# Kernel tuning notes

Hardware: AMD Instinct MI355X
Metric: run time of the kernel (lower is better)

The kernel has to match this reference:

```python
import jax, jax.numpy as jnp
import numpy as np
import math

HEADS = 16
HIDDEN = 2048
D_K = HIDDEN // HEADS
BATCH = 2
SEQ = 2048
ROPE_THETA = 10000.0


def make_freqs_cis(seq_len, d_k, theta=ROPE_THETA):
    # Llama rotary frequencies; returned as (seq, d_k//2, 2) = (cos, sin)
    inv_freq = 1.0 / (theta ** (np.arange(0, d_k, 2, dtype=np.float32) / d_k))
    t = np.arange(seq_len, dtype=np.float32)
    ang = np.outer(t, inv_freq)  # (seq, d_k//2)
    return jnp.asarray(np.stack([np.cos(ang), np.sin(ang)], axis=-1))


def setup_inputs() -> dict:
    key = jax.random.key(0)
    ks = jax.random.split(key, 5)
    scale = 1.0 / math.sqrt(HIDDEN)
    return {
        "x": jax.random.normal(ks[0], (BATCH, SEQ, HIDDEN), dtype=jnp.float32),
        "freqs_cis": make_freqs_cis(SEQ, D_K),
        "wq": jax.random.normal(ks[1], (HIDDEN, HIDDEN), dtype=jnp.float32) * scale,
        "wk": jax.random.normal(ks[2], (HIDDEN, HIDDEN), dtype=jnp.float32) * scale,
        "wv": jax.random.normal(ks[3], (HIDDEN, HIDDEN), dtype=jnp.float32) * scale,
        "wo": jax.random.normal(ks[4], (HIDDEN, HIDDEN), dtype=jnp.float32) * scale,
    }


def _apply_rope(t, cos, sin):
    # t: (B, S, h, d_k); cos/sin: (1, S, 1, d_k//2)
    B, S, h, dk = t.shape
    tp = t.reshape(B, S, h, dk // 2, 2)
    t0, t1 = tp[..., 0], tp[..., 1]
    r0 = t0 * cos - t1 * sin
    r1 = t0 * sin + t1 * cos
    return jnp.stack([r0, r1], axis=-1).reshape(B, S, h, dk)


def reference(x, freqs_cis, wq, wk, wv, wo):
    B, S, H = x.shape
    h, dk = HEADS, H // HEADS
    # nn.Linear(bias=False): y = x @ W.T
    q = (x @ wq.T).reshape(B, S, h, dk)
    k = (x @ wk.T).reshape(B, S, h, dk)
    v = (x @ wv.T).reshape(B, S, h, dk)
    cos = freqs_cis[None, :, None, :, 0]
    sin = freqs_cis[None, :, None, :, 1]
    q = _apply_rope(q, cos, sin)
    k = _apply_rope(k, cos, sin)
    # (B, h, S, dk)
    q = q.transpose(0, 2, 1, 3)
    k = k.transpose(0, 2, 1, 3)
    v = v.transpose(0, 2, 1, 3)
    scores = jnp.einsum("bhqd,bhkd->bhqk", q, k) / math.sqrt(dk)
    causal = jnp.tril(jnp.ones((S, S), dtype=bool))
    scores = jnp.where(causal[None, None], scores, -jnp.inf)
    attn = jax.nn.softmax(scores, axis=-1)
    out = jnp.einsum("bhqk,bhkd->bhqd", attn, v)
    out = out.transpose(0, 2, 1, 3).reshape(B, S, H)
    return out @ wo.T
```

## Files before the change

### kernel.cpp

```cpp
#include <hip/hip_runtime.h>

#define SEQ 2048
#define HID 2048
#define NH 16
#define DK 128
#define NTOK 4096

typedef __bf16 bf16x8 __attribute__((ext_vector_type(8)));
typedef float f32x4 __attribute__((ext_vector_type(4)));
typedef float f32x16 __attribute__((ext_vector_type(16)));
typedef unsigned int u32x4 __attribute__((ext_vector_type(4)));

__device__ __forceinline__ unsigned short f2bf(float f) {
  unsigned int u = __builtin_bit_cast(unsigned int, f);
  u += 0x7fffu + ((u >> 16) & 1u);
  return (unsigned short)(u >> 16);
}
__device__ __forceinline__ float bf2f(unsigned int lo16) {
  return __builtin_bit_cast(float, lo16 << 16);
}

__device__ __forceinline__ void async_cp16(const void* g, void* l) {
  __builtin_amdgcn_global_load_lds(
      (__attribute__((address_space(1))) void*)const_cast<void*>(g),
      (__attribute__((address_space(3))) void*)l, 16, 0, 0);
}

__global__ void convert_all_kernel(const float* __restrict__ x,
                                   const float* __restrict__ wq,
                                   const float* __restrict__ wk,
                                   const float* __restrict__ wv,
                                   const float* __restrict__ wo,
                                   const float* __restrict__ fc,
                                   unsigned short* __restrict__ xb,
                                   unsigned short* __restrict__ wqb,
                                   unsigned short* __restrict__ wkb,
                                   unsigned short* __restrict__ wvb,
                                   unsigned short* __restrict__ wob,
                                   unsigned int* __restrict__ fcb) {
  const int bid = blockIdx.x;
  if (bid >= 24576) {
    const int idx = (bid - 24576) * 256 + threadIdx.x;
    const int s = idx >> 6, d = idx & 63;
    const float2 cs = *(const float2*)(fc + s * 128 + 2 * d);
    fcb[idx] = (unsigned int)f2bf(cs.x) | ((unsigned int)f2bf(cs.y) << 16);
    return;
  }
  const float* src;
  unsigned short* dst;
  int base;
  if (bid < 8192) {
    src = x; dst = xb; base = bid;
  } else {
    const int t = (bid - 8192) >> 12;
    base = (bid - 8192) & 4095;
    src = (t == 0) ? wq : (t == 1) ? wk : (t == 2) ? wv : wo;
    dst = (t == 0) ? wqb : (t == 1) ? wkb : (t == 2) ? wvb : wob;
  }
  const int i = base * 256 + threadIdx.x;
  float4 v = ((const float4*)src)[i];
  ushort4 o;
  o.x = f2bf(v.x); o.y = f2bf(v.y); o.z = f2bf(v.z); o.w = f2bf(v.w);
  ((ushort4*)dst)[i] = o;
}

template<bool F32OUT>
__global__ __launch_bounds__(256, 2)
void gemm_bt_kernel(const unsigned short* __restrict__ A,
                    const unsigned short* __restrict__ B,
                    unsigned short* __restrict__ Ob,
                    float* __restrict__ Of,
                    const unsigned int* __restrict__ fcb,
                    const int mode) {
  __shared__ alignas(16) unsigned short As[128 * 64];
  __shared__ alignas(16) unsigned short Bs[128 * 64];

  const int bx = blockIdx.x, by = blockIdx.y;
  const int col0 = bx * 128;
  const int row0 = by * 128;

  const int tid = threadIdx.x;
  const int wave = tid >> 6, lane = tid & 63;
  const int quad = lane >> 4, r = lane & 15;
  const int wm = wave >> 1, wn = wave & 1;
  const int jbase = wave * 256 + lane;

  f32x4 acc[4][4] = {};

  for (int k0 = 0; k0 < HID; k0 += 64) {
    for (int t = 0; t < 4; ++t) {
      const int j = jbase + t * 64;
      const int m = j >> 3;
      const int gc = (j & 7) ^ (m & 7);
      async_cp16(A + (size_t)(row0 + m) * HID + k0 + gc * 8, As + j * 8);
      async_cp16(B + (size_t)(col0 + m) * HID + k0 + gc * 8, Bs + j * 8);
    }
    __syncthreads();
    for (int kk = 0; kk < 2; ++kk) {
      bf16x8 af[4], bfr[4];
      for (int mt = 0; mt < 4; ++mt) {
        const int m = wm * 64 + mt * 16 + r;
        const int slot = (kk * 4 + quad) ^ (m & 7);
        af[mt] = __builtin_bit_cast(bf16x8, *(const u32x4*)(As + m * 64 + slot * 8));
      }
      for (int nt = 0; nt < 4; ++nt) {
        const int n = wn * 64 + nt * 16 + r;
        const int slot = (kk * 4 + quad) ^ (n & 7);
        bfr[nt] = __builtin_bit_cast(bf16x8, *(const u32x4*)(Bs + n * 64 + slot * 8));
      }
      for (int mt = 0; mt < 4; ++mt)
        for (int nt = 0; nt < 4; ++nt)
          acc[mt][nt] = __builtin_amdgcn_mfma_f32_16x16x32_bf16(
              af[mt], bfr[nt], acc[mt][nt], 0, 0, 0);
    }
    __syncthreads();
  }

  if (!F32OUT && mode == 2) {
    for (int mt = 0; mt < 4; ++mt) {
      const int row = row0 + wm * 64 + mt * 16 + quad * 4;
      const int b = row >> 11, s = row & (SEQ - 1);
      for (int nt = 0; nt < 4; ++nt) {
        const int col = col0 + wn * 64 + nt * 16 + r;
        ushort4 pk;
        pk.x = f2bf(acc[mt][nt][0]);
        pk.y = f2bf(acc[mt][nt][1]);
        pk.z = f2bf(acc[mt][nt][2]);
        pk.w = f2bf(acc[mt][nt][3]);
        *(ushort4*)(Ob + ((size_t)(b * HID + col)) * SEQ + s) = pk;
      }
    }
    return;
  }

  if (!F32OUT) {
    const float qs = (mode == 0) ? 0.12751743f : 1.0f;
    for (int mt = 0; mt < 4; ++mt) {
      const int row = row0 + wm * 64 + mt * 16 + quad * 4;
      for (int nt = 0; nt < 4; ++nt) {
        const int col = col0 + wn * 64 + nt * 16 + r;
        const int d = (wn * 64 + nt * 16 + r) >> 1;
        for (int v = 0; v < 4; ++v) {
          const int s = (row + v) & (SEQ - 1);
          const unsigned int u = fcb[s * 64 + d];
          const float c = bf2f(u & 0xffffu), sn = bf2f(u >> 16);
          const float val = acc[mt][nt][v];
          const float par = __shfl_xor(val, 1, 64);
          const float res = (r & 1) ? (par * sn + val * c)
                                    : (val * c - par * sn);
          Ob[(size_t)(row + v) * HID + col] = f2bf(res * qs);
        }
      }
    }
    return;
  }

  for (int mt = 0; mt < 4; ++mt) {
    const int row = row0 + wm * 64 + mt * 16 + quad * 4;
    for (int nt = 0; nt < 4; ++nt) {
      const int col = col0 + wn * 64 + nt * 16 + r;
      for (int v = 0; v < 4; ++v)
        Of[(size_t)(row + v) * HID + col] = acc[mt][nt][v];
    }
  }
}

__global__ __launch_bounds__(256, 2)
void flash_attn_kernel(const unsigned short* __restrict__ Qb,
                       const unsigned short* __restrict__ Kb,
                       const unsigned short* __restrict__ VtG,
                       unsigned short* __restrict__ Ob) {
  __shared__ alignas(16) unsigned short Ks[64 * 128];
  __shared__ alignas(16) unsigned short Vs[128 * 64];
  __shared__ float Ml[4][64];

  const int bid = blockIdx.x;
  const int local = bid >> 3;
  const int bx = local >> 2;
  const int bh = (bid & 7) * 4 + (local & 3);
  const int tid = threadIdx.x, wave = tid >> 6, lane = tid & 63;
  const int l31 = lane & 31, hl = lane >> 5;
  const int qgrp = wave >> 1, ksub = wave & 1;
  const int tokbase = (bh >> 4) * SEQ;
  const int hh = bh & 15;

  const float NEG = -30000.f;

  auto stage = [&](int kt) {
#pragma unroll
    for (int t = 0; t < 4; ++t) {
      const int j = t * 256 + tid;
      const int n = j >> 4, slot = j & 15;
      const int gc = slot ^ (n & 15);
      async_cp16(Kb + (size_t)(tokbase + kt * 64 + n) * HID + hh * DK + gc * 8,
                 Ks + j * 8);
    }
#pragma unroll
    for (int t = 0; t < 4; ++t) {
      const int j = t * 256 + tid;
      const int d = j >> 3, slot = j & 7;
      const int gc = slot ^ (d & 7);
      async_cp16(VtG + (size_t)(bh * DK + d) * SEQ + kt * 64 + gc * 8,
                 Vs + j * 8);
    }
  };

  for (int phase = 0; phase < 2; ++phase) {
    const int qt = phase ? (31 - bx) : bx;
    const int q0 = qt * 64;
    const int qloc = qgrp * 32 + l31;

    u32x4 qf[8];
    {
      const unsigned short* qrow =
          Qb + (size_t)(tokbase + q0 + qloc) * HID + hh * DK;
#pragma unroll
      for (int ks = 0; ks < 8; ++ks)
        qf[ks] = *(const u32x4*)(qrow + ks * 16 + hl * 8);
    }

    f32x16 o[4] = {};
    float m_i = NEG, l_i = 0.f;

    for (int kt = 0; kt <= qt; ++kt) {
      stage(kt);
      __syncthreads();

      f32x16 s = {};
      const unsigned short* krow = Ks + (size_t)(ksub * 32 + l31) * 128;
      __builtin_amdgcn_s_setprio(1);
#pragma unroll
      for (int ks = 0; ks < 8; ++ks) {
        const int slot = (ks * 2 + hl) ^ (lane & 15);
        const u32x4 kf = *(const u32x4*)(krow + slot * 8);
        s = __builtin_amdgcn_mfma_f32_32x32x16_bf16(
            __builtin_bit_cast(bf16x8, kf),
            __builtin_bit_cast(bf16x8, qf[ks]), s, 0, 0, 0);
      }
      __builtin_amdgcn_s_setprio(0);

      float sv[16];
#pragma unroll
      for (int r = 0; r < 16; ++r) sv[r] = s[r];
      if (kt == qt) {
#pragma unroll
        for (int r = 0; r < 16; ++r) {
          const int kloc = ksub * 32 + (r & 3) + 8 * (r >> 2) + 4 * hl;
          if (kloc > qloc) sv[r] = NEG;
        }
      }

      float t0 = fmaxf(fmaxf(sv[0], sv[1]), sv[2]);
      float t1 = fmaxf(fmaxf(sv[3], sv[4]), sv[5]);
      float t2 = fmaxf(fmaxf(sv[6], sv[7]), sv[8]);
      float t3 = fmaxf(fmaxf(sv[9], sv[10]), sv[11]);
      float t4 = fmaxf(fmaxf(sv[12], sv[13]), sv[14]);
      float mx = fmaxf(fmaxf(fmaxf(t0, t1), t2),
                       fmaxf(fmaxf(t3, t4), sv[15]));
      mx = fmaxf(mx, __shfl_xor(mx, 32, 64));

      if (!__all(mx <= m_i + 8.f)) {
        const float mnew = fmaxf(m_i, mx);
        const float al = exp2f(m_i - mnew);
        m_i = mnew;
        l_i *= al;
#pragma unroll
        for (int dt = 0; dt < 4; ++dt)
#pragma unroll
          for (int r = 0; r < 16; ++r) o[dt][r] *= al;
      }

      float p[16];
      float rs = 0.f;
#pragma unroll
      for (int r = 0; r < 16; ++r) {
        p[r] = exp2f(sv[r] - m_i);
        rs += p[r];
      }
      l_i += rs + __shfl_xor(rs, 32, 64);

      u32x4 af[2];
#pragma unroll
      for (int kk = 0; kk < 2; ++kk) {
        unsigned int a, b2, c2, d2;
        asm("v_cvt_pk_bf16_f32 %0, %1, %2"
            : "=v"(a) : "v"(p[8 * kk + 0]), "v"(p[8 * kk + 1]));
        asm("v_cvt_pk_bf16_f32 %0, %1, %2"
            : "=v"(b2) : "v"(p[8 * kk + 2]), "v"(p[8 * kk + 3]));
        asm("v_cvt_pk_bf16_f32 %0, %1, %2"
            : "=v"(c2) : "v"(p[8 * kk + 4]), "v"(p[8 * kk + 5]));
        asm("v_cvt_pk_bf16_f32 %0, %1, %2"
            : "=v"(d2) : "v"(p[8 * kk + 6]), "v"(p[8 * kk + 7]));
        asm("v_permlane32_swap_b32 %0, %1" : "+v"(a), "+v"(c2));
        asm("v_permlane32_swap_b32 %0, %1" : "+v"(b2), "+v"(d2));
        u32x4 t = {a, b2, c2, d2};
        af[kk] = t;
      }

      __builtin_amdgcn_s_setprio(1);
#pragma unroll
      for (int kk = 0; kk < 2; ++kk)
#pragma unroll
        for (int dt = 0; dt < 4; ++dt) {
          const int d = dt * 32 + l31;
          const int slot = (ksub * 4 + kk * 2 + hl) ^ (d & 7);
          const u32x4 vv = *(const u32x4*)(Vs + (size_t)d * 64 + slot * 8);
          o[dt] = __builtin_amdgcn_mfma_f32_32x32x16_bf16(
              __builtin_bit_cast(bf16x8, af[kk]),
              __builtin_bit_cast(bf16x8, vv), o[dt], 0, 0, 0);
        }
      __builtin_amdgcn_s_setprio(0);

      __syncthreads();
    }

    float* obuf = (float*)(qgrp == 0 ? (void*)Ks : (void*)Vs);
    if (ksub == 1) {
#pragma unroll
      for (int dt = 0; dt < 4; ++dt)
#pragma unroll
        for (int r = 0; r < 16; ++r) {
          const int qr = (r & 3) + 8 * (r >> 2) + 4 * hl;
          obuf[qr * 128 + dt * 32 + l31] = o[dt][r];
        }
    }
    if (lane < 32) {
      Ml[wave][lane] = m_i;
      Ml[wave][32 + lane] = l_i;
    }
    __syncthreads();
    if (ksub == 0) {
      float f0[16], f1[16];
#pragma unroll
      for (int r = 0; r < 16; ++r) {
        const int qr = (r & 3) + 8 * (r >> 2) + 4 * hl;
        const float m0 = Ml[wave][qr];
        const float l0 = Ml[wave][32 + qr];
        const float m1 = Ml[wave + 1][qr];
        const float l1 = Ml[wave + 1][32 + qr];
        const float mm = fmaxf(m0, m1);
        const float a0 = exp2f(m0 - mm);
        const float a1 = exp2f(m1 - mm);
        const float li = 1.f / (l0 * a0 + l1 * a1);
        f0[r] = a0 * li;
        f1[r] = a1 * li;
      }
#pragma unroll
      for (int dt = 0; dt < 4; ++dt)
#pragma unroll
        for (int r = 0; r < 16; ++r) {
          const int qr = (r & 3) + 8 * (r >> 2) + 4 * hl;
          const float om =
              o[dt][r] * f0[r] + obuf[qr * 128 + dt * 32 + l31] * f1[r];
          Ob[(size_t)(tokbase + q0 + qgrp * 32 + qr) * HID + hh * DK +
             dt * 32 + l31] = f2bf(om);
        }
    }
    __syncthreads();
  }
}

extern "C" void kernel_launch(void* const* d_in, const int* in_sizes, int n_in,
                              void* d_out, int out_size, void* d_ws, size_t ws_size,
                              hipStream_t stream) {
  const float* x  = (const float*)d_in[0];
  const float* fc = (const float*)d_in[1];
  const float* wq = (const float*)d_in[2];
  const float* wk = (const float*)d_in[3];
  const float* wv = (const float*)d_in[4];
  const float* wo = (const float*)d_in[5];
  float* out = (float*)d_out;

  unsigned short* xb  = (unsigned short*)d_ws;
  unsigned short* wqb = xb  + (size_t)NTOK * HID;
  unsigned short* wkb = wqb + (size_t)HID * HID;
  unsigned short* wvb = wkb + (size_t)HID * HID;
  unsigned short* wob = wvb + (size_t)HID * HID;
  unsigned short* qb  = wob + (size_t)HID * HID;
  unsigned short* kb  = qb  + (size_t)NTOK * HID;
  unsigned short* vtb = kb  + (size_t)NTOK * HID;
  unsigned short* ab  = vtb + (size_t)NTOK * HID;
  unsigned int*   fcb = (unsigned int*)(ab + (size_t)NTOK * HID);

  convert_all_kernel<<<24576 + 512, 256, 0, stream>>>(
      x, wq, wk, wv, wo, fc, xb, wqb, wkb, wvb, wob, fcb);

  gemm_bt_kernel<false><<<dim3(16, 32), 256, 0, stream>>>(
      xb, wqb, qb, nullptr, fcb, 0);
  gemm_bt_kernel<false><<<dim3(16, 32), 256, 0, stream>>>(
      xb, wkb, kb, nullptr, fcb, 1);
  gemm_bt_kernel<false><<<dim3(16, 32), 256, 0, stream>>>(
      xb, wvb, vtb, nullptr, fcb, 2);

  flash_attn_kernel<<<dim3(512), 256, 0, stream>>>(qb, kb, vtb, ab);

  gemm_bt_kernel<true><<<dim3(16, 32), 256, 0, stream>>>(
      ab, wob, nullptr, out, fcb, 0);
}
```

Before: 363.0 us.

## Double flash-attention KV tile to 128 keys and skip fully masked sub-tiles

The flash attention loop now stages 128 keys of K and V per iteration instead of 64, which halves the number of barrier-synchronised iterations. Each wave computes two 32-key score blocks and skips work when its 64-key half lies entirely above the causal diagonal. This cuts barrier and staging overhead per key, but doubles LDS use to about 64KB per block. That may limit residency with launch_bounds(256,2), and it adds masked wasted work on the diagonal tiles.

```diff
diff --git a/kernel.cpp b/kernel.cpp
--- a/kernel.cpp
+++ b/kernel.cpp
@@ -170,8 +170,8 @@
                        const unsigned short* __restrict__ Kb,
                        const unsigned short* __restrict__ VtG,
                        unsigned short* __restrict__ Ob) {
-  __shared__ alignas(16) unsigned short Ks[64 * 128];
-  __shared__ alignas(16) unsigned short Vs[128 * 64];
+  __shared__ alignas(16) unsigned short Ks[128 * 128];
+  __shared__ alignas(16) unsigned short Vs[128 * 128];
   __shared__ float Ml[4][64];
 
   const int bid = blockIdx.x;
@@ -188,19 +188,19 @@
 
   auto stage = [&](int kt) {
 #pragma unroll
-    for (int t = 0; t < 4; ++t) {
+    for (int t = 0; t < 8; ++t) {
       const int j = t * 256 + tid;
       const int n = j >> 4, slot = j & 15;
       const int gc = slot ^ (n & 15);
-      async_cp16(Kb + (size_t)(tokbase + kt * 64 + n) * HID + hh * DK + gc * 8,
+      async_cp16(Kb + (size_t)(tokbase + kt * 128 + n) * HID + hh * DK + gc * 8,
                  Ks + j * 8);
     }
 #pragma unroll
-    for (int t = 0; t < 4; ++t) {
+    for (int t = 0; t < 8; ++t) {
       const int j = t * 256 + tid;
-      const int d = j >> 3, slot = j & 7;
-      const int gc = slot ^ (d & 7);
-      async_cp16(VtG + (size_t)(bh * DK + d) * SEQ + kt * 64 + gc * 8,
+      const int d = j >> 4, slot = j & 15;
+      const int gc = slot ^ (d & 15);
+      async_cp16(VtG + (size_t)(bh * DK + d) * SEQ + kt * 128 + gc * 8,
                  Vs + j * 8);
     }
   };
@@ -209,6 +209,7 @@
     const int qt = phase ? (31 - bx) : bx;
     const int q0 = qt * 64;
     const int qloc = qgrp * 32 + l31;
+    const int nt = (qt >> 1) + 1;
 
     u32x4 qf[8];
     {
@@ -222,94 +223,118 @@
     f32x16 o[4] = {};
     float m_i = NEG, l_i = 0.f;
 
-    for (int kt = 0; kt <= qt; ++kt) {
+    for (int kt = 0; kt < nt; ++kt) {
       stage(kt);
       __syncthreads();
 
-      f32x16 s = {};
-      const unsigned short* krow = Ks + (size_t)(ksub * 32 + l31) * 128;
-      __builtin_amdgcn_s_setprio(1);
-#pragma unroll
-      for (int ks = 0; ks < 8; ++ks) {
-        const int slot = (ks * 2 + hl) ^ (lane & 15);
-        const u32x4 kf = *(const u32x4*)(krow + slot * 8);
-        s = __builtin_amdgcn_mfma_f32_32x32x16_bf16(
-            __builtin_bit_cast(bf16x8, kf),
-            __builtin_bit_cast(bf16x8, qf[ks]), s, 0, 0, 0);
-      }
-      __builtin_amdgcn_s_setprio(0);
-
-      float sv[16];
-#pragma unroll
-      for (int r = 0; r < 16; ++r) sv[r] = s[r];
-      if (kt == qt) {
-#pragma unroll
-        for (int r = 0; r < 16; ++r) {
-          const int kloc = ksub * 32 + (r & 3) + 8 * (r >> 2) + 4 * hl;
-          if (kloc > qloc) sv[r] = NEG;
-        }
-      }
-
-      float t0 = fmaxf(fmaxf(sv[0], sv[1]), sv[2]);
-      float t1 = fmaxf(fmaxf(sv[3], sv[4]), sv[5]);
-      float t2 = fmaxf(fmaxf(sv[6], sv[7]), sv[8]);
-      float t3 = fmaxf(fmaxf(sv[9], sv[10]), sv[11]);
-      float t4 = fmaxf(fmaxf(sv[12], sv[13]), sv[14]);
-      float mx = fmaxf(fmaxf(fmaxf(t0, t1), t2),
-                       fmaxf(fmaxf(t3, t4), sv[15]));
-      mx = fmaxf(mx, __shfl_xor(mx, 32, 64));
-
-      if (!__all(mx <= m_i + 8.f)) {
-        const float mnew = fmaxf(m_i, mx);
-        const float al = exp2f(m_i - mnew);
-        m_i = mnew;
-        l_i *= al;
-#pragma unroll
-        for (int dt = 0; dt < 4; ++dt)
-#pragma unroll
-          for (int r = 0; r < 16; ++r) o[dt][r] *= al;
-      }
-
-      float p[16];
-      float rs = 0.f;
-#pragma unroll
-      for (int r = 0; r < 16; ++r) {
-        p[r] = exp2f(sv[r] - m_i);
-        rs += p[r];
-      }
-      l_i += rs + __shfl_xor(rs, 32, 64);
-
-      u32x4 af[2];
-#pragma unroll
-      for (int kk = 0; kk < 2; ++kk) {
-        unsigned int a, b2, c2, d2;
-        asm("v_cvt_pk_bf16_f32 %0, %1, %2"
-            : "=v"(a) : "v"(p[8 * kk + 0]), "v"(p[8 * kk + 1]));
-        asm("v_cvt_pk_bf16_f32 %0, %1, %2"
-            : "=v"(b2) : "v"(p[8 * kk + 2]), "v"(p[8 * kk + 3]));
-        asm("v_cvt_pk_bf16_f32 %0, %1, %2"
-            : "=v"(c2) : "v"(p[8 * kk + 4]), "v"(p[8 * kk + 5]));
-        asm("v_cvt_pk_bf16_f32 %0, %1, %2"
-            : "=v"(d2) : "v"(p[8 * kk + 6]), "v"(p[8 * kk + 7]));
-        asm("v_permlane32_swap_b32 %0, %1" : "+v"(a), "+v"(c2));
-        asm("v_permlane32_swap_b32 %0, %1" : "+v"(b2), "+v"(d2));
-        u32x4 t = {a, b2, c2, d2};
-        af[kk] = t;
-      }
-
-      __builtin_amdgcn_s_setprio(1);
-#pragma unroll
-      for (int kk = 0; kk < 2; ++kk)
-#pragma unroll
-        for (int dt = 0; dt < 4; ++dt) {
-          const int d = dt * 32 + l31;
-          const int slot = (ksub * 4 + kk * 2 + hl) ^ (d & 7);
-          const u32x4 vv = *(const u32x4*)(Vs + (size_t)d * 64 + slot * 8);
-          o[dt] = __builtin_amdgcn_mfma_f32_32x32x16_bf16(
-              __builtin_bit_cast(bf16x8, af[kk]),
-              __builtin_bit_cast(bf16x8, vv), o[dt], 0, 0, 0);
-        }
-      __builtin_amdgcn_s_setprio(0);
+      const bool dead = (kt * 128 + ksub * 64) > (q0 + qgrp * 32 + 31);
+      if (!dead) {
+        f32x16 s0 = {}, s1 = {};
+        const unsigned short* kr0 = Ks + (size_t)(ksub * 64 + l31) * 128;
+        const unsigned short* kr1 = kr0 + 32 * 128;
+        __builtin_amdgcn_s_setprio(1);
+#pragma unroll
+        for (int ks = 0; ks < 8; ++ks) {
+          const int slot = (ks * 2 + hl) ^ (l31 & 15);
+          const u32x4 k0 = *(const u32x4*)(kr0 + slot * 8);
+          const u32x4 k1 = *(const u32x4*)(kr1 + slot * 8);
+          s0 = __builtin_amdgcn_mfma_f32_32x32x16_bf16(
+              __builtin_bit_cast(bf16x8, k0),
+              __builtin_bit_cast(bf16x8, qf[ks]), s0, 0, 0, 0);
+          s1 = __builtin_amdgcn_mfma_f32_32x32x16_bf16(
+              __builtin_bit_cast(bf16x8, k1),
+              __builtin_bit_cast(bf16x8, qf[ks]), s1, 0, 0, 0);
+        }
+        __builtin_amdgcn_s_setprio(0);
+
+        float sv[32];
+#pragma unroll
+        for (int r = 0; r < 16; ++r) { sv[r] = s0[r]; sv[16 + r] = s1[r]; }
+        if (kt == nt - 1) {
+#pragma unroll
+          for (int c = 0; c < 2; ++c)
+#pragma unroll
+            for (int r = 0; r < 16; ++r) {
+              const int key = kt * 128 + ksub * 64 + c * 32 +
+                              (r & 3) + 8 * (r >> 2) + 4 * hl;
+              if (key > q0 + qloc) sv[c * 16 + r] = NEG;
+            }
+        }
+
+        float a0 = fmaxf(fmaxf(sv[0], sv[1]), sv[2]);
+        float a1 = fmaxf(fmaxf(sv[3], sv[4]), sv[5]);
+        float a2 = fmaxf(fmaxf(sv[6], sv[7]), sv[8]);
+        float a3 = fmaxf(fmaxf(sv[9], sv[10]), sv[11]);
+        float a4 = fmaxf(fmaxf(sv[12], sv[13]), sv[14]);
+        float a5 = fmaxf(fmaxf(sv[15], sv[16]), sv[17]);
+        float a6 = fmaxf(fmaxf(sv[18], sv[19]), sv[20]);
+        float a7 = fmaxf(fmaxf(sv[21], sv[22]), sv[23]);
+        float a8 = fmaxf(fmaxf(sv[24], sv[25]), sv[26]);
+        float a9 = fmaxf(fmaxf(sv[27], sv[28]), sv[29]);
+        float b0 = fmaxf(fmaxf(a0, a1), a2);
+        float b1 = fmaxf(fmaxf(a3, a4), a5);
+        float b2 = fmaxf(fmaxf(a6, a7), a8);
+        float b3 = fmaxf(fmaxf(a9, sv[30]), sv[31]);
+        float mx = fmaxf(fmaxf(b0, b1), fmaxf(b2, b3));
+        mx = fmaxf(mx, __shfl_xor(mx, 32, 64));
+
+        if (!__all(mx <= m_i + 8.f)) {
+          const float mnew = fmaxf(m_i, mx);
+          const float al = exp2f(m_i - mnew);
+          m_i = mnew;
+          l_i *= al;
+#pragma unroll
+          for (int dt = 0; dt < 4; ++dt)
+#pragma unroll
+            for (int r = 0; r < 16; ++r) o[dt][r] *= al;
+        }
+
+        float rs = 0.f;
+#pragma unroll
+        for (int r = 0; r < 32; ++r) {
+          sv[r] = exp2f(sv[r] - m_i);
+          rs += sv[r];
+        }
+        l_i += rs + __shfl_xor(rs, 32, 64);
+
+        u32x4 af[2][2];
+#pragma unroll
+        for (int c = 0; c < 2; ++c)
+#pragma unroll
+          for (int kk = 0; kk < 2; ++kk) {
+            const int b = c * 16 + kk * 8;
+            unsigned int pa, pb, pc, pd;
+            asm("v_cvt_pk_bf16_f32 %0, %1, %2"
+                : "=v"(pa) : "v"(sv[b + 0]), "v"(sv[b + 1]));
+            asm("v_cvt_pk_bf16_f32 %0, %1, %2"
+                : "=v"(pb) : "v"(sv[b + 2]), "v"(sv[b + 3]));
+            asm("v_cvt_pk_bf16_f32 %0, %1, %2"
+                : "=v"(pc) : "v"(sv[b + 4]), "v"(sv[b + 5]));
+            asm("v_cvt_pk_bf16_f32 %0, %1, %2"
+                : "=v"(pd) : "v"(sv[b + 6]), "v"(sv[b + 7]));
+            asm("v_permlane32_swap_b32 %0, %1" : "+v"(pa), "+v"(pc));
+            asm("v_permlane32_swap_b32 %0, %1" : "+v"(pb), "+v"(pd));
+            u32x4 t = {pa, pb, pc, pd};
+            af[c][kk] = t;
+          }
+
+        __builtin_amdgcn_s_setprio(1);
+#pragma unroll
+        for (int c = 0; c < 2; ++c)
+#pragma unroll
+          for (int kk = 0; kk < 2; ++kk)
+#pragma unroll
+            for (int dt = 0; dt < 4; ++dt) {
+              const int d = dt * 32 + l31;
+              const int idx = ksub * 8 + c * 4 + kk * 2 + hl;
+              const int slot = idx ^ (d & 15);
+              const u32x4 vv = *(const u32x4*)(Vs + (size_t)d * 128 + slot * 8);
+              o[dt] = __builtin_amdgcn_mfma_f32_32x32x16_bf16(
+                  __builtin_bit_cast(bf16x8, af[c][kk]),
+                  __builtin_bit_cast(bf16x8, vv), o[dt], 0, 0, 0);
+            }
+        __builtin_amdgcn_s_setprio(0);
+      }
 
       __syncthreads();
     }
@@ -319,7 +344,7 @@
 #pragma unroll
       for (int dt = 0; dt < 4; ++dt)
 #pragma unroll
-        for (int r = 0; r < 16; ++r) {
+      for (int r = 0; r < 16; ++r) {
           const int qr = (r & 3) + 8 * (r >> 2) + 4 * hl;
           obuf[qr * 128 + dt * 32 + l31] = o[dt][r];
         }
```

New measurement: 367.1 us. About the same (+1.1%).
